# Performance work log

Measured on AMD Instinct MI355X. Metric: run time of the kernel, lower is better.

The kernel has to match this reference:

```python
import jax, jax.numpy as jnp
import numpy as np

B, C, H, W, NA = 2, 512, 25, 25, 9
A = H * W * NA  # 5625 anchors
PROB_T = 0.5
OVL_T = 0.5


def _make_anchors():
    ys, xs = np.meshgrid(np.arange(H), np.arange(W), indexing='ij')
    cx = (xs + 0.5) / W
    cy = (ys + 0.5) / H
    boxes = []
    for s in (0.1, 0.2, 0.4):
        for r in (0.5, 1.0, 2.0):
            w = s * np.sqrt(r)
            h = s / np.sqrt(r)
            boxes.append(np.stack([cx - w / 2, cy - h / 2, cx + w / 2, cy + h / 2], -1))
    anc = np.stack(boxes, axis=2)  # [H, W, 9, 4] matches [B,H,W,9*4] reshape order
    return jnp.asarray(anc.reshape(-1, 4), jnp.float32)


def setup_inputs() -> dict:
    key = jax.random.key(0)
    ks = jax.random.split(key, 4)
    x = jax.random.normal(ks[0], (B, C, H, W), jnp.float32)
    conv_w = jax.random.normal(ks[1], (512, 512, 3, 3), jnp.float32) * (1.0 / np.sqrt(512 * 9))
    conv_b = jnp.zeros((512,), jnp.float32)
    reg_w = jax.random.normal(ks[2], (36, 512), jnp.float32) * 0.02
    reg_b = jnp.zeros((36,), jnp.float32)
    cls_w = jax.random.normal(ks[3], (9, 512), jnp.float32) * 0.05
    cls_b = jnp.zeros((9,), jnp.float32)
    anchors = _make_anchors()
    return {"x": x, "conv_w": conv_w, "conv_b": conv_b, "reg_w": reg_w,
            "reg_b": reg_b, "cls_w": cls_w, "cls_b": cls_b, "anchors": anchors}


def reference(x, conv_w, conv_b, reg_w, reg_b, cls_w, cls_b, anchors):
    # --- RPN forward ---
    h = jax.lax.conv_general_dilated(x, conv_w, (1, 1), 'SAME',
                                     dimension_numbers=('NCHW', 'OIHW', 'NCHW'))
    h = jax.nn.relu(h + conv_b[None, :, None, None])
    box = jnp.einsum('bchw,oc->bhwo', h, reg_w) + reg_b  # [B,H,W,36] (== permute NHWC)
    cls = jnp.einsum('bchw,oc->bhwo', h, cls_w) + cls_b  # [B,H,W,9]
    offsets = box.reshape(B, A, 4)
    logits = cls.reshape(B, A)
    # --- detect: sigmoid + threshold ---
    probs = jax.nn.sigmoid(logits)
    valid = probs > PROB_T
    # --- box decode: gcxgcy -> cxcy -> xy (SSD-style, anchors given in xy) ---
    a_cx = (anchors[:, 0] + anchors[:, 2]) * 0.5
    a_cy = (anchors[:, 1] + anchors[:, 3]) * 0.5
    a_w = anchors[:, 2] - anchors[:, 0]
    a_h = anchors[:, 3] - anchors[:, 1]
    cx = offsets[..., 0] * a_w / 10.0 + a_cx
    cy = offsets[..., 1] * a_h / 10.0 + a_cy
    bw = jnp.exp(offsets[..., 2] / 5.0) * a_w
    bh = jnp.exp(offsets[..., 3] / 5.0) * a_h
    boxes = jnp.stack([cx - bw / 2, cy - bh / 2, cx + bw / 2, cy + bh / 2], -1)  # [B,A,4]
    # --- sort descending by score; invalid anchors sorted last and pre-suppressed ---
    sort_key = jnp.where(valid, probs, -1.0)
    order = jnp.argsort(-sort_key, axis=-1)
    sb = jnp.take_along_axis(boxes, order[..., None], axis=1)  # sorted boxes
    ss = jnp.take_along_axis(probs, order, axis=1)             # sorted scores
    sv = jnp.take_along_axis(valid, order, axis=1)             # sorted validity

    def per_image(b, v):
        x1, y1, x2, y2 = b[:, 0], b[:, 1], b[:, 2], b[:, 3]
        area = (x2 - x1) * (y2 - y1)
        iw = jnp.clip(jnp.minimum(x2[:, None], x2[None, :]) - jnp.maximum(x1[:, None], x1[None, :]), 0.0)
        ih = jnp.clip(jnp.minimum(y2[:, None], y2[None, :]) - jnp.maximum(y1[:, None], y1[None, :]), 0.0)
        inter = iw * ih
        ov = inter / (area[:, None] + area[None, :] - inter)  # [A,A] Jaccard
        sup0 = (~v).astype(jnp.int32)  # invalid anchors never considered

        def body(i, sup):
            cand = jnp.maximum(sup, (ov[i] > OVL_T).astype(jnp.int32)).at[i].set(0)
            return jnp.where(sup[i] > 0, sup, cand)  # skip if already suppressed

        sup = jax.lax.fori_loop(0, A, body, sup0)
        return (1 - sup) * v.astype(jnp.int32)

    keep = jax.vmap(per_image)(sb, sv)  # [B,A] 1 = kept detection
    return jnp.concatenate([sb, ss[..., None], keep[..., None].astype(jnp.float32)], -1)  # [B,A,6]
```

## Files before the change

### kernel.cpp

```cpp
#include <hip/hip_runtime.h>
#include <cstdint>
#include <cstddef>

#define AA 5625
#define MROWS 5760
#define ND 24

__global__ __launch_bounds__(256) void k_wt(const float* __restrict__ cw,
                                            float* __restrict__ wt,
                                            int* __restrict__ Vcnt) {
  if (blockIdx.x == 0 && threadIdx.x < 2) Vcnt[threadIdx.x] = 0;
  __shared__ float t[64][65];
  int kb = (blockIdx.x % 72) * 64;
  int ob = (blockIdx.x / 72) * 64;
  int col = threadIdx.x & 63;
  int rr  = threadIdx.x >> 6;
#pragma unroll
  for (int it = 0; it < 16; ++it) {
    int row = rr + it * 4;
    t[row][col] = cw[(size_t)(ob + row) * 4608 + kb + col];
  }
  __syncthreads();
#pragma unroll
  for (int it = 0; it < 16; ++it) {
    int row = rr + it * 4;
    wt[(size_t)(kb + row) * 512 + ob + col] = t[col][row];
  }
}

__global__ void k_xpad(const float* __restrict__ x, float* __restrict__ xp) {
  int n = blockIdx.x * 256 + threadIdx.x;
  if (n >= 884736) return;
  int c = n & 31;
  int r = (n >> 5) % 27;
  int rest = (n >> 5) / 27;
  float v = 0.f;
  int oy = r - 1, ox = c - 1;
  if (oy >= 0 && oy < 25 && ox >= 0 && ox < 25)
    v = x[(size_t)rest * 625 + oy * 25 + ox];
  xp[n] = v;
}

__global__ __launch_bounds__(256) void k_conv(const float* __restrict__ wt,
                                              const float* __restrict__ xp,
                                              double* __restrict__ hpart,
                                              int Kper) {
  int cpx = gridDim.x >> 3;
  int flat = blockIdx.x;
  int logical = (flat & 7) * cpx + (flat >> 3);
  int sharer = logical % 10;
  int s      = logical / 10;
  int Nt = s & 3;
  int ks = s >> 2;
  int b  = sharer / 5;
  int Mt = sharer % 5;

  int tid = threadIdx.x;
  int m0  = Mt * 128;
  int oc0 = Nt * 128;
  int R  = (tid >> 6) * 32 + ((tid >> 4) & 3) * 8;
  int cb = 2 * (tid & 15);

  __shared__ __align__(16) float As[2][18][128];
  __shared__ __align__(16) float Bs[2][18][128];

  double acc[8][8];
#pragma unroll
  for (int i = 0; i < 8; ++i)
#pragma unroll
    for (int j = 0; j < 8; ++j) acc[i][j] = 0.0;

  int kbase = ks * Kper;
  int nchunk = Kper / 18;

  int ldso[9];
  int boff[9];
  int aoff[9];
#pragma unroll
  for (int t = 0; t < 9; ++t) {
    int s2 = tid + 256 * t;
    int row = s2 >> 7, col = s2 & 127;
    ldso[t] = row * 128 + col;
    boff[t] = row * 512 + oc0 + col;
    int m = m0 + col;
    bool av = (m < 625);
    int mm = av ? m : 0;
    int icl = (row >= 9) ? 1 : 0;
    int tap = row - 9 * icl;
    int dy = tap / 3, dx = tap - 3 * dy;
    int yy = mm / 25, xx = mm - yy * 25;
    int ao = (icl * 27 + yy + dy) * 32 + xx + dx;
    aoff[t] = av ? ao : -1;
  }
  const float* wbase = wt + (size_t)kbase * 512;
  const float* abase = xp + (size_t)(b * 512 + kbase / 9) * 864;

  float rA[9], rB[9];

#define LOADCH(CH) {                                                          \
    int k0e = (CH) * (18 * 512);                                              \
    int a0e = (CH) * (2 * 864);                                               \
    _Pragma("unroll")                                                         \
    for (int t = 0; t < 9; ++t) {                                             \
      rB[t] = wbase[k0e + boff[t]];                                           \
      rA[t] = (aoff[t] >= 0) ? abase[a0e + aoff[t]] : 0.f;                    \
    } }
#define WRITECH(BUF) {                                                        \
    _Pragma("unroll")                                                         \
    for (int t = 0; t < 9; ++t) {                                             \
      ((float*)Bs[BUF])[ldso[t]] = rB[t];                                     \
      ((float*)As[BUF])[ldso[t]] = rA[t];                                     \
    } }

  LOADCH(0);
  WRITECH(0);
  __syncthreads();

  for (int ch = 0; ch < nchunk; ++ch) {
    int cur = ch & 1, nxt = cur ^ 1;
    int chn = (ch + 1 < nchunk) ? (ch + 1) : (nchunk - 1);
    LOADCH(chn);
#pragma unroll 2
    for (int kk = 0; kk < 18; ++kk) {
      float4 a0 = *(const float4*)&As[cur][kk][R];
      float4 a1 = *(const float4*)&As[cur][kk][R + 4];
      float2 b0 = *(const float2*)&Bs[cur][kk][cb];
      float2 b1 = *(const float2*)&Bs[cur][kk][cb + 32];
      float2 b2 = *(const float2*)&Bs[cur][kk][cb + 64];
      float2 b3 = *(const float2*)&Bs[cur][kk][cb + 96];
      double ad[8] = {(double)a0.x, (double)a0.y, (double)a0.z, (double)a0.w,
                      (double)a1.x, (double)a1.y, (double)a1.z, (double)a1.w};
      double bd[8] = {(double)b0.x, (double)b0.y, (double)b1.x, (double)b1.y,
                      (double)b2.x, (double)b2.y, (double)b3.x, (double)b3.y};
#pragma unroll
      for (int i = 0; i < 8; ++i)
#pragma unroll
        for (int j = 0; j < 8; ++j) acc[i][j] += ad[i] * bd[j];
    }
    if (ch + 1 < nchunk) {
      __syncthreads();
      WRITECH(nxt);
      __syncthreads();
    }
  }

  double* hb = hpart + ((size_t)(ks * 2 + b) * 625) * 512 + oc0 + cb;
#pragma unroll
  for (int i = 0; i < 8; ++i) {
    int mm = m0 + R + i;
    if (mm < 625) {
      double* p = hb + (size_t)mm * 512;
#pragma unroll
      for (int r = 0; r < 4; ++r) {
        double2 v; v.x = acc[i][2 * r]; v.y = acc[i][2 * r + 1];
        *(double2*)(p + 32 * r) = v;
      }
    }
  }
#undef LOADCH
#undef WRITECH
}

__device__ __forceinline__ double shfl_down_d(double x, int off) {
  long long v = __double_as_longlong(x);
  int lo = __shfl_down((int)(unsigned int)(v & 0xffffffffLL), off);
  int hi = __shfl_down((int)(v >> 32), off);
  return __longlong_as_double(((long long)hi << 32) | (unsigned int)lo);
}

__global__ __launch_bounds__(256) void k_heads(
    const double* __restrict__ hpart, const float* __restrict__ conv_b,
    const float* __restrict__ reg_w, const float* __restrict__ reg_b,
    const float* __restrict__ cls_w, const float* __restrict__ cls_b,
    const float* __restrict__ anchors, float* __restrict__ boxesraw,
    float* __restrict__ probs, unsigned long long* __restrict__ keys,
    unsigned int* __restrict__ rank, int nsplit) {
  int pos = blockIdx.x % 625;
  int b   = blockIdx.x / 625;
  int tid = threadIdx.x;
  __shared__ double hv[512];
  __shared__ double res[45];
  for (int c = tid; c < 512; c += 256) {
    double s = 0.0;
    for (int k = 0; k < nsplit; ++k)
      s += hpart[(((size_t)k * 2 + b) * 625 + pos) * 512 + c];
    s += (double)conv_b[c];
    hv[c] = s > 0.0 ? s : 0.0;
  }
  __syncthreads();
  int wv = tid >> 6, l = tid & 63;
  for (int o = wv; o < 45; o += 4) {
    const float* wrow = (o < 36) ? (reg_w + (size_t)o * 512)
                                 : (cls_w + (size_t)(o - 36) * 512);
    double s = 0.0;
#pragma unroll
    for (int kk = 0; kk < 8; ++kk)
      s += hv[l + kk * 64] * (double)wrow[l + kk * 64];
#pragma unroll
    for (int d = 32; d > 0; d >>= 1) s += shfl_down_d(s, d);
    if (l == 0) res[o] = s + (double)((o < 36) ? reg_b[o] : cls_b[o - 36]);
  }
  __syncthreads();
  if (tid < 9) {
    int na = tid;
    int a = pos * 9 + na;
    double o0 = res[na * 4 + 0], o1 = res[na * 4 + 1];
    double o2 = res[na * 4 + 2], o3 = res[na * 4 + 3];
    double logit = res[36 + na];
    float4 anc = *(const float4*)(anchors + (size_t)a * 4);
    double a_cx = ((double)anc.x + (double)anc.z) * 0.5;
    double a_cy = ((double)anc.y + (double)anc.w) * 0.5;
    double a_w = (double)anc.z - (double)anc.x;
    double a_h = (double)anc.w - (double)anc.y;
    double cx = o0 * a_w / 10.0 + a_cx;
    double cy = o1 * a_h / 10.0 + a_cy;
    double bw = exp(o2 / 5.0) * a_w;
    double bh = exp(o3 / 5.0) * a_h;
    float4 box = make_float4((float)(cx - bw / 2.0), (float)(cy - bh / 2.0),
                             (float)(cx + bw / 2.0), (float)(cy + bh / 2.0));
    size_t ga = (size_t)b * AA + a;
    *(float4*)(boxesraw + ga * 4) = box;
    float p = (float)(1.0 / (1.0 + exp(-logit)));
    probs[ga] = p;
    bool valid = p > 0.5f;
    float f = -(valid ? p : -1.0f);
    unsigned int u = __float_as_uint(f);
    u = (u & 0x80000000u) ? ~u : (u | 0x80000000u);
    keys[ga] = (((unsigned long long)u) << 32) | (unsigned int)a;
    rank[ga] = 0u;
  }
}

__global__ __launch_bounds__(256) void k_count(
    const unsigned long long* __restrict__ keys, unsigned int* __restrict__ rank) {
  int b = blockIdx.z;
  int i = blockIdx.x * 256 + threadIdx.x;
  __shared__ unsigned long long sj[1024];
  unsigned long long my = (i < AA) ? keys[(size_t)b * AA + i] : 0ULL;
  int j0 = blockIdx.y * 1024;
  for (int jj = threadIdx.x; jj < 1024; jj += 256) {
    int j = j0 + jj;
    sj[jj] = (j < AA) ? keys[(size_t)b * AA + j] : ~0ULL;
  }
  __syncthreads();
  int cnt = 0;
#pragma unroll 8
  for (int jj = 0; jj < 1024; ++jj) cnt += (sj[jj] < my) ? 1 : 0;
  if (i < AA && cnt) atomicAdd(&rank[(size_t)b * AA + i], (unsigned)cnt);
}

__global__ void k_perm(const unsigned long long* __restrict__ keys,
                       const unsigned int* __restrict__ rank,
                       unsigned int* __restrict__ perm, int* __restrict__ Vcnt) {
  int idx = blockIdx.x * 256 + threadIdx.x;
  if (idx >= 2 * AA) return;
  int b = idx / AA, i = idx - b * AA;
  unsigned long long k = keys[idx];
  unsigned int r = rank[idx];
  perm[(size_t)b * AA + r] = (unsigned)i;
  if (!(k >> 63)) atomicAdd(&Vcnt[b], 1);
}

__global__ void k_assembly(const unsigned int* __restrict__ perm,
                           const float* __restrict__ boxesraw,
                           const float* __restrict__ probs,
                           float* __restrict__ out, float4* __restrict__ sb4) {
  int idx = blockIdx.x * 256 + threadIdx.x;
  if (idx >= 2 * AA) return;
  int b = idx / AA;
  unsigned int pa = perm[idx];
  float4 bx = *(const float4*)(boxesraw + ((size_t)b * AA + pa) * 4);
  float p = probs[(size_t)b * AA + pa];
  float* o = out + (size_t)idx * 6;
  o[0] = bx.x; o[1] = bx.y; o[2] = bx.z; o[3] = bx.w; o[4] = p; o[5] = 0.f;
  sb4[idx] = bx;
}

__global__ __launch_bounds__(256) void k_maskT(const float4* __restrict__ sb4,
                                               const int* __restrict__ Vcnt,
                                               ulonglong2* __restrict__ maskT) {
  int b = blockIdx.y;
  int V = Vcnt[b];
  int i = blockIdx.x * 4 + (threadIdx.x >> 6);
  if (i >= V) return;
  int lane = threadIdx.x & 63;
  float4 bif = sb4[(size_t)b * AA + i];
  double bix = bif.x, biy = bif.y, biz = bif.z, biw = bif.w;
  double ai = (biz - bix) * (biw - biy);
  unsigned long long lo = 0, hi = 0;
#pragma unroll 4
  for (int w = 0; w < 88; ++w) {
    int j = w * 64 + lane;
    int jc = (j < AA) ? j : (AA - 1);
    float4 c = sb4[(size_t)b * AA + jc];
    double aj = ((double)c.z - (double)c.x) * ((double)c.w - (double)c.y);
    double iw = fmin(biz, (double)c.z) - fmax(bix, (double)c.x);
    double ih = fmin(biw, (double)c.w) - fmax(biy, (double)c.y);
    iw = iw > 0.0 ? iw : 0.0;
    ih = ih > 0.0 ? ih : 0.0;
    double inter = iw * ih;
    bool bit = (inter + inter > ai + aj - inter) && (j != i) && (j < AA);
    unsigned long long bb = bit ? 1ULL : 0ULL;
    if (w < 64) lo |= bb << w;
    else        hi |= bb << (w - 64);
  }
  ulonglong2 v; v.x = lo; v.y = hi;
  maskT[((size_t)b * MROWS + i) * 64 + lane] = v;
}

#define NMS_STEP(RING, I)                                                     \
  {                                                                           \
    int i = (I);                                                              \
    if (i < V) {                                                              \
      int w = i >> 6, t = i & 63;                                             \
      if (t == 0) {                                                           \
        unsigned long long cbit = (w < 64) ? (colLo >> w) : (colHi >> (w - 64)); \
        supw = __ballot((int)(cbit & 1ULL));                                  \
      }                                                                       \
      if (!((supw >> t) & 1ULL)) {                                            \
        colLo |= RING.x; colHi |= RING.y;                                     \
        unsigned long long cbit = (w < 64) ? (colLo >> w) : (colHi >> (w - 64)); \
        supw = __ballot((int)(cbit & 1ULL));                                  \
        if (lane == 0) out[((size_t)b * AA + i) * 6 + 5] = 1.0f;              \
      }                                                                       \
    }                                                                         \
  }

__global__ __launch_bounds__(64) void k_nms(const ulonglong2* __restrict__ maskT,
                                            const int* __restrict__ Vcnt,
                                            float* __restrict__ out) {
  int b = blockIdx.x;
  int lane = threadIdx.x;
  int V = Vcnt[b];
  const ulonglong2* mt = maskT + (size_t)b * MROWS * 64;
  unsigned long long colLo = 0, colHi = 0, supw = 0;
  ulonglong2 ra[ND], rb[ND];
#pragma unroll
  for (int j = 0; j < ND; ++j) ra[j] = mt[(size_t)j * 64 + lane];
#pragma unroll
  for (int j = 0; j < ND; ++j) rb[j] = mt[(size_t)(ND + j) * 64 + lane];
  for (int base = 0; base < V; base += 2 * ND) {
#pragma unroll
    for (int j = 0; j < ND; ++j) NMS_STEP(ra[j], base + j);
#pragma unroll
    for (int j = 0; j < ND; ++j) ra[j] = mt[(size_t)(base + 2 * ND + j) * 64 + lane];
#pragma unroll
    for (int j = 0; j < ND; ++j) NMS_STEP(rb[j], base + ND + j);
#pragma unroll
    for (int j = 0; j < ND; ++j) rb[j] = mt[(size_t)(base + 3 * ND + j) * 64 + lane];
  }
}
#undef NMS_STEP

extern "C" void kernel_launch(void* const* d_in, const int* in_sizes, int n_in,
                              void* d_out, int out_size, void* d_ws, size_t ws_size,
                              hipStream_t stream) {
  const float* x      = (const float*)d_in[0];
  const float* conv_w = (const float*)d_in[1];
  const float* conv_b = (const float*)d_in[2];
  const float* reg_w  = (const float*)d_in[3];
  const float* reg_b  = (const float*)d_in[4];
  const float* cls_w  = (const float*)d_in[5];
  const float* cls_b  = (const float*)d_in[6];
  const float* anchors= (const float*)d_in[7];
  float* out = (float*)d_out;
  char* ws = (char*)d_ws;

  size_t off = 0;
  auto alloc = [&](size_t bytes) {
    size_t o = off;
    off += (bytes + 255) & ~(size_t)255;
    return o;
  };
  size_t o_wt   = alloc(4608ULL * 512 * 4);
  size_t o_xp   = alloc(884736ULL * 4);
  size_t o_box  = alloc(2ULL * AA * 4 * 4);
  size_t o_prob = alloc(2ULL * AA * 4);
  size_t o_keys = alloc(2ULL * AA * 8);
  size_t o_rank = alloc(2ULL * AA * 4);
  size_t o_perm = alloc(2ULL * AA * 4);
  size_t o_sb4  = alloc(2ULL * AA * 16);
  size_t o_V    = alloc(256);
  size_t o_maskT= alloc(2ULL * MROWS * 64 * 16);
  size_t fixed = off;

  int nsplit = 1;
  const int cands[5] = {16, 8, 4, 2, 1};
  for (int ci = 0; ci < 5; ++ci) {
    size_t need = fixed + (size_t)cands[ci] * 2 * 625 * 512 * 8;
    if (need <= ws_size) { nsplit = cands[ci]; break; }
  }
  size_t o_hp = alloc((size_t)nsplit * 2 * 625 * 512 * 8);

  float* wtp   = (float*)(ws + o_wt);
  float* xpp   = (float*)(ws + o_xp);
  float* boxp  = (float*)(ws + o_box);
  float* probp = (float*)(ws + o_prob);
  unsigned long long* keysp = (unsigned long long*)(ws + o_keys);
  unsigned int* rankp = (unsigned int*)(ws + o_rank);
  unsigned int* permp = (unsigned int*)(ws + o_perm);
  float4* sb4p = (float4*)(ws + o_sb4);
  int* Vp      = (int*)(ws + o_V);
  ulonglong2* maskTp = (ulonglong2*)(ws + o_maskT);
  double* hpp  = (double*)(ws + o_hp);

  k_wt<<<dim3(576), dim3(256), 0, stream>>>(conv_w, wtp, Vp);
  k_xpad<<<dim3(3456), dim3(256), 0, stream>>>(x, xpp);
  k_conv<<<dim3(40 * nsplit), dim3(256), 0, stream>>>(wtp, xpp, hpp, 4608 / nsplit);
  k_heads<<<dim3(1250), dim3(256), 0, stream>>>(hpp, conv_b, reg_w, reg_b,
                                                cls_w, cls_b, anchors, boxp,
                                                probp, keysp, rankp, nsplit);
  k_count<<<dim3(22, 6, 2), dim3(256), 0, stream>>>(keysp, rankp);
  k_perm<<<dim3(44), dim3(256), 0, stream>>>(keysp, rankp, permp, Vp);
  k_assembly<<<dim3(44), dim3(256), 0, stream>>>(permp, boxp, probp, out, sb4p);
  k_maskT<<<dim3(1407, 2), dim3(256), 0, stream>>>(sb4p, Vp, maskTp);
  k_nms<<<dim3(2), dim3(64), 0, stream>>>(maskTp, Vp, out);
}
```

Before: 545.8 us.

## Halve conv N-tile to 64 channels and stream NMS mask rows via 16-deep prefetch ring

The FP64-accumulating conv GEMM tile shrinks from 128x128 to 128x64 output channels. This doubles the grid and halves per-thread accumulators, to raise occupancy and block count at the cost of reloading the activation tile twice as often. The NMS kernel drops its two 24-row register batches for a 16-entry rolling ring. Each step issues the load for row i+16 right after consuming row i, which lowers register pressure and keeps loads continuously in flight.

New measurement: 531.6 us. 2.6% less time.

```diff
diff --git a/kernel.cpp b/kernel.cpp
--- a/kernel.cpp
+++ b/kernel.cpp
@@ -4,7 +4,6 @@
 
 #define AA 5625
 #define MROWS 5760
-#define ND 24
 
 __global__ __launch_bounds__(256) void k_wt(const float* __restrict__ cw,
                                             float* __restrict__ wt,
@@ -50,38 +49,35 @@
   int logical = (flat & 7) * cpx + (flat >> 3);
   int sharer = logical % 10;
   int s      = logical / 10;
-  int Nt = s & 3;
-  int ks = s >> 2;
+  int Nt = s & 7;
+  int ks = s >> 3;
   int b  = sharer / 5;
   int Mt = sharer % 5;
 
   int tid = threadIdx.x;
   int m0  = Mt * 128;
-  int oc0 = Nt * 128;
+  int oc0 = Nt * 64;
   int R  = (tid >> 6) * 32 + ((tid >> 4) & 3) * 8;
   int cb = 2 * (tid & 15);
 
   __shared__ __align__(16) float As[2][18][128];
-  __shared__ __align__(16) float Bs[2][18][128];
-
-  double acc[8][8];
+  __shared__ __align__(16) float Bs[2][18][64];
+
+  double acc[8][4];
 #pragma unroll
   for (int i = 0; i < 8; ++i)
 #pragma unroll
-    for (int j = 0; j < 8; ++j) acc[i][j] = 0.0;
+    for (int j = 0; j < 4; ++j) acc[i][j] = 0.0;
 
   int kbase = ks * Kper;
   int nchunk = Kper / 18;
 
-  int ldso[9];
-  int boff[9];
-  int aoff[9];
+  int ldsoA[9], aoff[9];
 #pragma unroll
   for (int t = 0; t < 9; ++t) {
     int s2 = tid + 256 * t;
     int row = s2 >> 7, col = s2 & 127;
-    ldso[t] = row * 128 + col;
-    boff[t] = row * 512 + oc0 + col;
+    ldsoA[t] = row * 128 + col;
     int m = m0 + col;
     bool av = (m < 625);
     int mm = av ? m : 0;
@@ -92,25 +88,40 @@
     int ao = (icl * 27 + yy + dy) * 32 + xx + dx;
     aoff[t] = av ? ao : -1;
   }
+  int ldsoB[5], boffB[5];
+  bool bval[5];
+#pragma unroll
+  for (int t = 0; t < 5; ++t) {
+    int s2 = tid + 256 * t;
+    bval[t] = (s2 < 1152);
+    int s2c = bval[t] ? s2 : 0;
+    int row = s2c >> 6, col = s2c & 63;
+    ldsoB[t] = row * 64 + col;
+    boffB[t] = row * 512 + oc0 + col;
+  }
   const float* wbase = wt + (size_t)kbase * 512;
   const float* abase = xp + (size_t)(b * 512 + kbase / 9) * 864;
 
-  float rA[9], rB[9];
+  float rA[9], rB[5];
 
 #define LOADCH(CH) {                                                          \
     int k0e = (CH) * (18 * 512);                                              \
     int a0e = (CH) * (2 * 864);                                               \
     _Pragma("unroll")                                                         \
-    for (int t = 0; t < 9; ++t) {                                             \
-      rB[t] = wbase[k0e + boff[t]];                                           \
+    for (int t = 0; t < 9; ++t)                                               \
       rA[t] = (aoff[t] >= 0) ? abase[a0e + aoff[t]] : 0.f;                    \
-    } }
+    _Pragma("unroll")                                                         \
+    for (int t = 0; t < 5; ++t)                                               \
+      rB[t] = bval[t] ? wbase[k0e + boffB[t]] : 0.f;                          \
+  }
 #define WRITECH(BUF) {                                                        \
     _Pragma("unroll")                                                         \
-    for (int t = 0; t < 9; ++t) {                                             \
-      ((float*)Bs[BUF])[ldso[t]] = rB[t];                                     \
-      ((float*)As[BUF])[ldso[t]] = rA[t];                                     \
-    } }
+    for (int t = 0; t < 9; ++t)                                               \
+      ((float*)As[BUF])[ldsoA[t]] = rA[t];                                    \
+    _Pragma("unroll")                                                         \
+    for (int t = 0; t < 5; ++t)                                               \
+      if (bval[t]) ((float*)Bs[BUF])[ldsoB[t]] = rB[t];                       \
+  }
 
   LOADCH(0);
   WRITECH(0);
@@ -126,16 +137,13 @@
       float4 a1 = *(const float4*)&As[cur][kk][R + 4];
       float2 b0 = *(const float2*)&Bs[cur][kk][cb];
       float2 b1 = *(const float2*)&Bs[cur][kk][cb + 32];
-      float2 b2 = *(const float2*)&Bs[cur][kk][cb + 64];
-      float2 b3 = *(const float2*)&Bs[cur][kk][cb + 96];
       double ad[8] = {(double)a0.x, (double)a0.y, (double)a0.z, (double)a0.w,
                       (double)a1.x, (double)a1.y, (double)a1.z, (double)a1.w};
-      double bd[8] = {(double)b0.x, (double)b0.y, (double)b1.x, (double)b1.y,
-                      (double)b2.x, (double)b2.y, (double)b3.x, (double)b3.y};
+      double bd[4] = {(double)b0.x, (double)b0.y, (double)b1.x, (double)b1.y};
 #pragma unroll
       for (int i = 0; i < 8; ++i)
 #pragma unroll
-        for (int j = 0; j < 8; ++j) acc[i][j] += ad[i] * bd[j];
+        for (int j = 0; j < 4; ++j) acc[i][j] += ad[i] * bd[j];
     }
     if (ch + 1 < nchunk) {
       __syncthreads();
@@ -150,11 +158,10 @@
     int mm = m0 + R + i;
     if (mm < 625) {
       double* p = hb + (size_t)mm * 512;
-#pragma unroll
-      for (int r = 0; r < 4; ++r) {
-        double2 v; v.x = acc[i][2 * r]; v.y = acc[i][2 * r + 1];
-        *(double2*)(p + 32 * r) = v;
-      }
+      double2 v0; v0.x = acc[i][0]; v0.y = acc[i][1];
+      double2 v1; v1.x = acc[i][2]; v1.y = acc[i][3];
+      *(double2*)p        = v0;
+      *(double2*)(p + 32) = v1;
     }
   }
 #undef LOADCH
@@ -308,9 +315,9 @@
   maskT[((size_t)b * MROWS + i) * 64 + lane] = v;
 }
 
-#define NMS_STEP(RING, I)                                                     \
+#define NMS_STEP(Q, J)                                                        \
   {                                                                           \
-    int i = (I);                                                              \
+    int i = base + (J);                                                       \
     if (i < V) {                                                              \
       int w = i >> 6, t = i & 63;                                             \
       if (t == 0) {                                                           \
@@ -318,12 +325,13 @@
         supw = __ballot((int)(cbit & 1ULL));                                  \
       }                                                                       \
       if (!((supw >> t) & 1ULL)) {                                            \
-        colLo |= RING.x; colHi |= RING.y;                                     \
+        colLo |= Q.x; colHi |= Q.y;                                           \
         unsigned long long cbit = (w < 64) ? (colLo >> w) : (colHi >> (w - 64)); \
         supw = __ballot((int)(cbit & 1ULL));                                  \
         if (lane == 0) out[((size_t)b * AA + i) * 6 + 5] = 1.0f;              \
       }                                                                       \
     }                                                                         \
+    Q = mt[(size_t)(i + 16) * 64 + lane];                                     \
   }
 
 __global__ __launch_bounds__(64) void k_nms(const ulonglong2* __restrict__ maskT,
@@ -334,20 +342,19 @@
   int V = Vcnt[b];
   const ulonglong2* mt = maskT + (size_t)b * MROWS * 64;
   unsigned long long colLo = 0, colHi = 0, supw = 0;
-  ulonglong2 ra[ND], rb[ND];
-#pragma unroll
-  for (int j = 0; j < ND; ++j) ra[j] = mt[(size_t)j * 64 + lane];
-#pragma unroll
-  for (int j = 0; j < ND; ++j) rb[j] = mt[(size_t)(ND + j) * 64 + lane];
-  for (int base = 0; base < V; base += 2 * ND) {
-#pragma unroll
-    for (int j = 0; j < ND; ++j) NMS_STEP(ra[j], base + j);
-#pragma unroll
-    for (int j = 0; j < ND; ++j) ra[j] = mt[(size_t)(base + 2 * ND + j) * 64 + lane];
-#pragma unroll
-    for (int j = 0; j < ND; ++j) NMS_STEP(rb[j], base + ND + j);
-#pragma unroll
-    for (int j = 0; j < ND; ++j) rb[j] = mt[(size_t)(base + 3 * ND + j) * 64 + lane];
+  ulonglong2 q00 = mt[(size_t)0  * 64 + lane], q01 = mt[(size_t)1  * 64 + lane];
+  ulonglong2 q02 = mt[(size_t)2  * 64 + lane], q03 = mt[(size_t)3  * 64 + lane];
+  ulonglong2 q04 = mt[(size_t)4  * 64 + lane], q05 = mt[(size_t)5  * 64 + lane];
+  ulonglong2 q06 = mt[(size_t)6  * 64 + lane], q07 = mt[(size_t)7  * 64 + lane];
+  ulonglong2 q08 = mt[(size_t)8  * 64 + lane], q09 = mt[(size_t)9  * 64 + lane];
+  ulonglong2 q10 = mt[(size_t)10 * 64 + lane], q11 = mt[(size_t)11 * 64 + lane];
+  ulonglong2 q12 = mt[(size_t)12 * 64 + lane], q13 = mt[(size_t)13 * 64 + lane];
+  ulonglong2 q14 = mt[(size_t)14 * 64 + lane], q15 = mt[(size_t)15 * 64 + lane];
+  for (int base = 0; base < V; base += 16) {
+    NMS_STEP(q00, 0)  NMS_STEP(q01, 1)  NMS_STEP(q02, 2)  NMS_STEP(q03, 3)
+    NMS_STEP(q04, 4)  NMS_STEP(q05, 5)  NMS_STEP(q06, 6)  NMS_STEP(q07, 7)
+    NMS_STEP(q08, 8)  NMS_STEP(q09, 9)  NMS_STEP(q10, 10) NMS_STEP(q11, 11)
+    NMS_STEP(q12, 12) NMS_STEP(q13, 13) NMS_STEP(q14, 14) NMS_STEP(q15, 15)
   }
 }
 #undef NMS_STEP
@@ -406,7 +413,7 @@
 
   k_wt<<<dim3(576), dim3(256), 0, stream>>>(conv_w, wtp, Vp);
   k_xpad<<<dim3(3456), dim3(256), 0, stream>>>(x, xpp);
-  k_conv<<<dim3(40 * nsplit), dim3(256), 0, stream>>>(wtp, xpp, hpp, 4608 / nsplit);
+  k_conv<<<dim3(80 * nsplit), dim3(256), 0, stream>>>(wtp, xpp, hpp, 4608 / nsplit);
   k_heads<<<dim3(1250), dim3(256), 0, stream>>>(hpp, conv_b, reg_w, reg_b,
                                                 cls_w, cls_b, anchors, boxp,
                                                 probp, keysp, rankp, nsplit);
```
